# Kernel tuning notes

Measured on AMD Instinct MI355X. Metric: run time of the kernel, lower is better.

Reference implementation:

```python
import jax, jax.numpy as jnp
import numpy as np

N_BALLS = 256
BATCH = 128
N_STEPS = 100
MAX_EVENTS = 5
WORLD_W = 10.0
WORLD_H = 10.0
RADIUS = 0.1
HID = 64
DT = 0.05
INF = jnp.float32(1e30)

_II_np, _JJ_np = np.triu_indices(N_BALLS, 1)
_II = jnp.asarray(_II_np)
_JJ = jnp.asarray(_JJ_np)
# wall order: left, right, bottom, top (normals point into the box)
_WN = jnp.array([[1.0, 0.0], [-1.0, 0.0], [0.0, 1.0], [0.0, -1.0]], dtype=jnp.float32)
_WP = jnp.array([0.0, -WORLD_W, 0.0, -WORLD_H], dtype=jnp.float32)


def setup_inputs():
    key = jax.random.key(0)
    ks = jax.random.split(key, 6)
    pos = jax.random.uniform(ks[0], (BATCH, N_BALLS, 2), minval=0.5, maxval=9.5)
    vel = jax.random.normal(ks[1], (BATCH, N_BALLS, 2))
    state = jnp.concatenate([pos, vel], axis=-1)  # [B, N, 4]
    radii = jnp.full((N_BALLS,), RADIUS, dtype=jnp.float32)
    sc = 0.1
    W1 = jax.random.normal(ks[2], (HID, 2)) * sc
    b1 = jnp.zeros((HID,), jnp.float32)
    W2 = jax.random.normal(ks[3], (HID, HID)) * sc
    b2 = jnp.zeros((HID,), jnp.float32)
    W3 = jax.random.normal(ks[4], (1, HID)) * sc
    b3 = jnp.zeros((1,), jnp.float32)
    return {"state": state, "radii": radii, "W1": W1, "b1": b1, "W2": W2,
            "b2": b2, "W3": W3, "b3": b3, "dt": DT, "n_steps": N_STEPS}


def _detect(pos, vel, radii):
    # pos, vel: [N,2]; vectorized replacement of the Python O(N^2) loop.
    diff = pos[_JJ] - pos[_II]                       # [P,2]
    dist = jnp.linalg.norm(diff, axis=-1)            # [P]
    gap_b = dist - (radii[_II] + radii[_JJ])
    nhat = diff / (dist + 1e-8)[:, None]
    app_b = jnp.sum((vel[_JJ] - vel[_II]) * nhat, axis=-1)
    gb = jnp.where(app_b < 0, gap_b, INF)            # only approaching pairs
    r = radii
    gw = jnp.stack([pos[:, 0] - r, WORLD_W - pos[:, 0] - r,
                    pos[:, 1] - r, WORLD_H - pos[:, 1] - r], axis=-1)  # [N,4]
    vw = jnp.stack([vel[:, 0] < 0, vel[:, 0] > 0,
                    vel[:, 1] < 0, vel[:, 1] > 0], axis=-1)
    gw = jnp.where(vw, gw, INF)
    allg = jnp.concatenate([gb, gw.reshape(-1)])
    k = jnp.argmin(allg)
    P = gb.shape[0]
    is_ball = k < P
    gap = allg[k]
    bi = jnp.where(is_ball, k, 0)
    i_b, j_b = _II[bi], _JJ[bi]
    kw = jnp.where(is_ball, 0, k - P)
    i_w, wid = kw // 4, kw % 4
    return gap, is_ball, i_b, j_b, i_w, wid


def _apply_jump(s, i, j, W1, b1, W2, b2, W3, b3):
    pos, vel = s[..., :2], s[..., 2:]
    diff = pos[:, j] - pos[:, i]                               # [B,2]
    dist = jnp.maximum(jnp.linalg.norm(diff, axis=-1, keepdims=True), 1e-8)
    nhat = diff / dist
    app = jnp.sum((vel[:, j] - vel[:, i]) * nhat, axis=-1, keepdims=True)
    h = jnp.concatenate([dist, app], axis=-1)                  # [B,2]
    h = jax.nn.silu(h @ W1.T + b1)
    h = jax.nn.silu(h @ W2.T + b2)
    imp = (h @ W3.T + b3) * nhat                               # [B,2]
    vel_new = vel.at[:, i].add(imp).at[:, j].add(-imp)
    return jnp.concatenate([pos, vel_new], axis=-1)


def _apply_wall(s, i, wn, wp, r):
    pos, vel = s[..., :2], s[..., 2:]
    v, p = vel[:, i], pos[:, i]
    vn = jnp.sum(v * wn, axis=-1, keepdims=True)
    vel_new = vel.at[:, i].set(v - 2.0 * vn * wn)
    pn = jnp.sum(p * wn, axis=-1, keepdims=True)
    pen = jnp.maximum(wp + r - pn, 0.0)
    pos_new = pos.at[:, i].set(p + pen * wn)
    return jnp.concatenate([pos_new, vel_new], axis=-1)


def _rollout(state, radii, W1, b1, W2, b2, W3, b3, dt, n_steps):
    dt = jnp.float32(dt)

    def event_body(_, carry):
        curr, t_c, t_e, done = carry
        pos0, vel0 = curr[0, :, :2], curr[0, :, 2:]
        gap, is_ball, i_b, j_b, i_w, wid = _detect(pos0, vel0, radii)
        no_event = gap > 0.05
        n = pos0[j_b] - pos0[i_b]
        app_ball = -jnp.sum((vel0[j_b] - vel0[i_b]) * n / jnp.linalg.norm(n))
        app_wall = jnp.abs(jnp.max(vel0[i_w]))
        app = jnp.where(is_ball, app_ball, app_wall)
        t_ev = t_c + gap / jnp.maximum(app, 1e-6)
        # ZeroFlow is constant velocity -> dopri5 integrate is exact linear drift
        dte = jnp.where(t_ev > t_c + 1e-10, t_ev - t_c, 0.0)

        def apply_map(s):
            jm = _apply_jump(s, i_b, j_b, W1, b1, W2, b2, W3, b3)
            wm = _apply_wall(s, i_w, _WN[wid], _WP[wid], radii[i_w])
            return jnp.where(is_ball, jm, wm)

        state_a = apply_map(curr)                       # gap <= 0: jump now
        integ = curr.at[..., :2].add(curr[..., 2:] * dte)
        state_b = apply_map(integ)                      # 0 < gap: drift then jump
        act = (~done) & (~no_event)
        case_a = act & (gap <= 0)
        case_b = act & (gap > 0) & (app > 1e-6) & (t_ev < t_e)
        new_done = done | no_event | (act & (gap > 0) & ((app <= 1e-6) | (t_ev >= t_e)))
        new_curr = jnp.where(case_a, state_a, jnp.where(case_b, state_b, curr))
        new_t_c = jnp.where(case_b, t_ev, t_c)
        return new_curr, new_t_c, t_e, new_done

    def step(curr, step_idx):
        t_s = step_idx.astype(jnp.float32) * dt
        t_e = t_s + dt
        curr, t_c, _, _ = jax.lax.fori_loop(
            0, MAX_EVENTS, event_body, (curr, t_s, t_e, jnp.bool_(False)))
        dte = jnp.where(t_e > t_c + 1e-10, t_e - t_c, 0.0)
        curr = curr.at[..., :2].add(curr[..., 2:] * dte)
        return curr, curr

    _, traj = jax.lax.scan(step, state, jnp.arange(n_steps))
    return jnp.concatenate([state[None], traj], axis=0)   # [n_steps+1, B, N, 4]


def reference(state, radii, W1, b1, W2, b2, W3, b3, dt, n_steps):
    return _rollout(state, radii, W1, b1, W2, b2, W3, b3, dt, n_steps)
```

## Files before the change

kernel.cpp:

```cpp
#include <hip/hip_runtime.h>
#include <stdint.h>

#define NB 256
#define NBATCH 128
#define HID 64
#define MAXEV 5
#define MAXSTEPS 256
#define NT 43
#define NTILES 946
#define W2S 65
#define CAND_MAX 6144
#define CMARGIN 1.5f
#define NTHR 512
#define D2GATE 0.0626f

typedef unsigned long long u64;

__device__ __forceinline__ float bf2f(unsigned short u) {
    return __uint_as_float(((unsigned)u) << 16);
}
__device__ __forceinline__ unsigned short f2bf(float f) {
    unsigned u = __float_as_uint(f);
    u += 0x7FFFu + ((u >> 16) & 1u);
    return (unsigned short)(u >> 16);
}
__device__ __forceinline__ float rdin(const void* p, int idx, int bf) {
    return bf ? bf2f(((const unsigned short*)p)[idx]) : ((const float*)p)[idx];
}
__device__ __forceinline__ float silu_f(float x) {
    float s = __fdiv_rn(1.0f, __fadd_rn(1.0f, expf(-x)));
    return __fmul_rn(x, s);
}
__device__ __forceinline__ void lds_fence() {
    __builtin_amdgcn_wave_barrier();
    __threadfence_block();
    __builtin_amdgcn_wave_barrier();
}
__device__ __forceinline__ u64 shfl_down_u64(u64 v, int off) {
    unsigned lo = (unsigned)v, hi = (unsigned)(v >> 32);
    lo = __shfl_down(lo, off);
    hi = __shfl_down(hi, off);
    return (((u64)hi) << 32) | lo;
}
__device__ __forceinline__ unsigned fmap(float g) {
    unsigned u = __float_as_uint(g);
    unsigned m = (unsigned)(((int)u) >> 31) | 0x80000000u;
    return u ^ m;
}
__device__ __forceinline__ float funmap(unsigned sb) {
    unsigned u = (sb & 0x80000000u) ? (sb ^ 0x80000000u) : ~sb;
    return __uint_as_float(u);
}

__device__ __forceinline__ void append_agg(unsigned* list, int* counter, int cap, unsigned val) {
    u64 m = __ballot(1);
    int lane = (int)(threadIdx.x & 63);
    int ldr = (int)__builtin_ctzll(m);
    int pfx = (int)__builtin_popcountll(m & ((1ull << lane) - 1ull));
    int base = 0;
    if (lane == ldr) base = atomicAdd(counter, (int)__builtin_popcountll(m));
    base = __builtin_amdgcn_readfirstlane(base);
    int idx = base + pfx;
    if (idx < cap) list[idx] = val;
}

__device__ __forceinline__ u64 ball_key(const float4* ps, int i, int j,
                                        float dx, float dy, float d2,
                                        unsigned id, float rsum) {
    float4 A = ps[i], B = ps[j];
    float p1 = __fmul_rn(__fsub_rn(B.z, A.z), dx);
    float p2 = __fmul_rn(__fsub_rn(B.w, A.w), dy);
    float dot = __fadd_rn(p1, p2);
    float mag = __fadd_rn(fabsf(p1), fabsf(p2));
    bool appr;
    if (fabsf(dot) < __fmul_rn(1e-5f, mag)) {
        float dist = __fsqrt_rn(d2);
        float den = __fadd_rn(dist, 1e-8f);
        float ab = __fadd_rn(__fmul_rn(__fsub_rn(B.z, A.z), __fdiv_rn(dx, den)),
                             __fmul_rn(__fsub_rn(B.w, A.w), __fdiv_rn(dy, den)));
        appr = ab < 0.0f;
    } else {
        appr = dot < 0.0f;
    }
    if (!appr) return ~0ull;
    float gap = __fsub_rn(__fsqrt_rn(d2), rsum);
    return (((u64)fmap(gap)) << 17) | id;
}

__device__ void load_weights(float* w1, float* b1s, float* w2, float* b2s, float* w3, float* b3s,
                             const void* W1, const void* B1, const void* W2, const void* B2,
                             const void* W3, const void* B3, int bf, int tid, int nthr) {
    for (int k = tid; k < HID * 2; k += nthr) w1[k] = rdin(W1, k, bf);
    for (int k = tid; k < HID; k += nthr) {
        b1s[k] = rdin(B1, k, bf);
        b2s[k] = rdin(B2, k, bf);
        w3[k]  = rdin(W3, k, bf);
    }
    for (int k = tid; k < HID * HID; k += nthr) {
        int m = k >> 6, c = k & 63;
        w2[m * W2S + c] = rdin(W2, k, bf);
    }
    if (tid == 0) b3s[0] = rdin(B3, 0, bf);
}

__global__ void sniff_kernel(const unsigned short* st, int* ws) {
    __shared__ int ev;
    if (threadIdx.x == 0) ev = 0;
    __syncthreads();
    unsigned short u = st[threadIdx.x];
    int e = (u >> 7) & 0xFF;
    if (e >= 0x85) atomicOr(&ev, 1);
    __syncthreads();
    if (threadIdx.x == 0) ws[0] = ev ? 0 : 1;
}

__global__ void row0_kernel(const void* in, void* out, const int* ws) {
    int idx = blockIdx.x * blockDim.x + threadIdx.x;
    if (ws[0]) ((unsigned short*)out)[idx] = ((const unsigned short*)in)[idx];
    else       ((float*)out)[idx] = ((const float*)in)[idx];
}

__global__ __launch_bounds__(NTHR, 1) void sim_kernel(
    const void* in_state, const void* in_rad,
    const void* inW1, const void* inB1, const void* inW2, const void* inB2,
    const void* inW3, const void* inB3, const void* in_dt, const int* in_nsteps,
    void* out, const int* ws) {
    __shared__ float4 ps0[NB];
    __shared__ float4 psb[NB];
    __shared__ float2 pos2[NB];
    __shared__ float rad[NB];
    __shared__ float w1[HID * 2], b1s[HID], w2[HID * W2S], b2s[HID], w3s[HID], b3s[1];
    __shared__ float sc0[132], scb[132];
    __shared__ u64 redK[8];
    __shared__ float redF[4];
    __shared__ unsigned cand[CAND_MAX];
    __shared__ int candN;
    __shared__ int dI[4];
    __shared__ float dF[4];
    __shared__ int candF;
    __shared__ int rebF;

    int tid = threadIdx.x;
    int b = blockIdx.x;
    int bf = ws[0];

    if (tid < NB) {
        int base0 = tid * 4;
        float4 P;
        P.x = rdin(in_state, base0 + 0, bf);
        P.y = rdin(in_state, base0 + 1, bf);
        P.z = rdin(in_state, base0 + 2, bf);
        P.w = rdin(in_state, base0 + 3, bf);
        ps0[tid] = P;
        float2 p2v; p2v.x = P.x; p2v.y = P.y;
        pos2[tid] = p2v;
        int baseb = (b * NB + tid) * 4;
        float4 Q;
        Q.x = rdin(in_state, baseb + 0, bf);
        Q.y = rdin(in_state, baseb + 1, bf);
        Q.z = rdin(in_state, baseb + 2, bf);
        Q.w = rdin(in_state, baseb + 3, bf);
        psb[tid] = Q;
        rad[tid] = rdin(in_rad, tid, bf);
        float m2 = P.z * P.z + P.w * P.w;
        #pragma unroll
        for (int off = 32; off; off >>= 1) m2 = fmaxf(m2, __shfl_down(m2, off));
        if ((tid & 63) == 0) redF[tid >> 6] = m2;
    }
    load_weights(w1, b1s, w2, b2s, w3s, b3s, inW1, inB1, inW2, inB2, inW3, inB3, bf, tid, NTHR);
    if (tid == 0) { candN = 0; candF = 0; rebF = 1; }

    float dtv = rdin(in_dt, 0, bf);
    int NS = in_nsteps[0]; if (NS > MAXSTEPS) NS = MAXSTEPS; if (NS < 0) NS = 0;

    int i0a = -1, j0a = 0, i0b = -1, j0b = 0;
    {
        int T = tid;
        if (T < NTILES) {
            int rem = T, r = 0;
            while (rem >= NT - r) { rem -= NT - r; r++; }
            i0a = r * 6; j0a = (r + rem) * 6;
        }
        T = tid + NTHR;
        if (T < NTILES) {
            int rem = T, r = 0;
            while (rem >= NT - r) { rem -= NT - r; r++; }
            i0b = r * 6; j0b = (r + rem) * 6;
        }
    }
    __syncthreads();
    float rsum = __fadd_rn(rad[0], rad[0]);

    float thB = __fadd_rn(__fadd_rn(rsum, 0.05f), CMARGIN);
    float th2B = __fmul_rn(thB, thB);

    int nc = 0;
    bool candOvf = false;
    float used = 1e30f, vcap = 0.0f;

    for (int s = 0; s < NS; s++) {
        int rebuild = rebF;
        float t_s = __fmul_rn((float)s, dtv);
        float t_e = __fadd_rn(t_s, dtv);
        float t_c = t_s;
        if (tid < 64) {
            if (rebuild) {
                vcap = sqrtf(fmaxf(fmaxf(redF[0], redF[1]), fmaxf(redF[2], redF[3])));
                used = 0.0f;
            }
            used = __fadd_rn(used, __fmul_rn(__fmul_rn(2.0f, dtv), vcap));
            if (tid == 0 && rebuild) candF = 0;
        }

        for (int e = 0; e < MAXEV; e++) {
            u64 kC = ~0ull;
            bool fullscan = (e == 0) ? (rebuild != 0) : (candF != 0);
            bool doAppend = (e == 0) && rebuild;
            if (fullscan) {
                #pragma unroll
                for (int tt = 0; tt < 2; tt++) {
                    int I0 = tt ? i0b : i0a;
                    int J0 = tt ? j0b : j0a;
                    if (I0 < 0) continue;
                    float2 Pi[6], Pj[6];
                    #pragma unroll
                    for (int a = 0; a < 6; a++) {
                        int ii = I0 + a; ii = ii < NB ? ii : NB - 1;
                        int jj = J0 + a; jj = jj < NB ? jj : NB - 1;
                        Pi[a] = pos2[ii]; Pj[a] = pos2[jj];
                    }
                    #pragma unroll
                    for (int a = 0; a < 6; a++) {
                        int i = I0 + a;
                        #pragma unroll
                        for (int bb = 0; bb < 6; bb++) {
                            int j = J0 + bb;
                            bool ok = (i < NB) && (j < NB) && (j > i);
                            float dx = __fsub_rn(Pj[bb].x, Pi[a].x);
                            float dy = __fsub_rn(Pj[bb].y, Pi[a].y);
                            float d2 = __fadd_rn(__fmul_rn(dx, dx), __fmul_rn(dy, dy));
                            unsigned id = (unsigned)((i << 8) | j);
                            if (doAppend && ok && d2 < th2B)
                                append_agg(cand, &candN, CAND_MAX, id);
                            if (ok && d2 < D2GATE) {
                                u64 key = ball_key(ps0, i, j, dx, dy, d2, id, rsum);
                                kC = key < kC ? key : kC;
                            }
                        }
                    }
                }
            } else {
                for (int c = tid; c < nc; c += NTHR) {
                    unsigned id = cand[c];
                    int i = (int)(id >> 8), j = (int)(id & 255u);
                    float2 A = pos2[i], B = pos2[j];
                    float dx = __fsub_rn(B.x, A.x), dy = __fsub_rn(B.y, A.y);
                    float d2 = __fadd_rn(__fmul_rn(dx, dx), __fmul_rn(dy, dy));
                    if (d2 < D2GATE) {
                        u64 key = ball_key(ps0, i, j, dx, dy, d2, id, rsum);
                        kC = key < kC ? key : kC;
                    }
                }
            }
            {
                int ball = tid & 255, wsel = tid >> 8;
                float4 P = ps0[ball]; float r = rad[ball];
                #pragma unroll
                for (int q = 0; q < 2; q++) {
                    int w = wsel * 2 + q;
                    float g; bool valid;
                    if (w == 0)      { g = __fsub_rn(P.x, r); valid = P.z < 0.0f; }
                    else if (w == 1) { g = __fsub_rn(__fsub_rn(10.0f, P.x), r); valid = P.z > 0.0f; }
                    else if (w == 2) { g = __fsub_rn(P.y, r); valid = P.w < 0.0f; }
                    else             { g = __fsub_rn(__fsub_rn(10.0f, P.y), r); valid = P.w > 0.0f; }
                    if (valid) {
                        u64 key = (((u64)fmap(g)) << 17) | 0x10000u | (unsigned)(ball * 4 + w);
                        kC = key < kC ? key : kC;
                    }
                }
            }
            #pragma unroll
            for (int off = 32; off; off >>= 1) {
                u64 o = shfl_down_u64(kC, off);
                kC = o < kC ? o : kC;
            }
            if ((tid & 63) == 0) redK[tid >> 6] = kC;
            __syncthreads();

            if (e == 0 && rebuild) {
                int ct = candN;
                candOvf = ct > CAND_MAX;
                nc = candOvf ? CAND_MAX : ct;
            }

            float g_nx = 0, g_ny = 0, g_dist = 0, g_app = 0;
            float4 gA, gB;
            if (tid < 64) {
                u64 m = redK[0];
                #pragma unroll
                for (int q = 1; q < 8; q++) m = redK[q] < m ? redK[q] : m;
                int code_ = 0; float dteB_ = 0.0f, tcn_ = t_c;
                int ei_ = 0, ej_ = 0;
                if (m != ~0ull) {
                    bool is_ball = ((m >> 16) & 1ull) == 0;
                    unsigned id = (unsigned)(m & 0xFFFFull);
                    float gap = funmap((unsigned)(m >> 17));
                    int pi = (int)(id >> 8), pj = (int)(id & 255u);
                    int wb = (int)(id >> 2), ww = (int)(id & 3u);
                    ei_ = is_ball ? pi : wb;
                    ej_ = is_ball ? pj : ww;
                    if (!(gap > 0.05f)) {
                        float app;
                        if (is_ball) {
                            float4 A = ps0[pi], B = ps0[pj];
                            float dx = __fsub_rn(B.x, A.x), dy = __fsub_rn(B.y, A.y);
                            float nrm = __fsqrt_rn(__fadd_rn(__fmul_rn(dx, dx), __fmul_rn(dy, dy)));
                            float dvx = __fsub_rn(B.z, A.z), dvy = __fsub_rn(B.w, A.w);
                            app = -__fadd_rn(__fdiv_rn(__fmul_rn(dvx, dx), nrm),
                                             __fdiv_rn(__fmul_rn(dvy, dy), nrm));
                        } else {
                            float4 Wb = ps0[wb];
                            app = fabsf(fmaxf(Wb.z, Wb.w));
                        }
                        float t_ev = __fadd_rn(t_c, __fdiv_rn(gap, fmaxf(app, 1e-6f)));
                        if (gap <= 0.0f) {
                            code_ = is_ball ? 1 : 3;
                        } else if (app > 1e-6f && t_ev < t_e) {
                            code_ = is_ball ? 2 : 4;
                            dteB_ = (t_ev > __fadd_rn(t_c, 1e-10f)) ? __fsub_rn(t_ev, t_c) : 0.0f;
                            tcn_ = t_ev;
                        }
                    }
                }
                if (tid == 0) {
                    dI[0] = code_; dI[1] = ei_; dI[2] = ej_;
                    dF[0] = dteB_; dF[1] = tcn_;
                }
                if (code_ != 0 && code_ <= 2) {
                    float4 A = ps0[ei_], B = ps0[ej_];
                    if (code_ == 2) {
                        A.x = __fadd_rn(A.x, __fmul_rn(A.z, dteB_));
                        A.y = __fadd_rn(A.y, __fmul_rn(A.w, dteB_));
                        B.x = __fadd_rn(B.x, __fmul_rn(B.z, dteB_));
                        B.y = __fadd_rn(B.y, __fmul_rn(B.w, dteB_));
                    }
                    gA = A; gB = B;
                    float dx = __fsub_rn(B.x, A.x), dy = __fsub_rn(B.y, A.y);
                    float nrm = __fsqrt_rn(__fadd_rn(__fmul_rn(dx, dx), __fmul_rn(dy, dy)));
                    float dist = fmaxf(nrm, 1e-8f);
                    g_nx = __fdiv_rn(dx, dist); g_ny = __fdiv_rn(dy, dist);
                    g_dist = dist;
                    float dvx = __fsub_rn(B.z, A.z), dvy = __fsub_rn(B.w, A.w);
                    g_app = __fadd_rn(__fmul_rn(dvx, g_nx), __fmul_rn(dvy, g_ny));
                }
            }
            __syncthreads();

            int code = dI[0];
            if (code == 0) break;
            int ei = dI[1], ejw = dI[2];
            float dteB = dF[0];
            t_c = dF[1];
            bool integ = (code == 2) || (code == 4);

            if (code <= 2) {
                if (tid < 64) {
                    float a = __fadd_rn(__fadd_rn(__fmul_rn(g_dist, w1[2 * tid]),
                                                  __fmul_rn(g_app, w1[2 * tid + 1])), b1s[tid]);
                    sc0[4 + tid] = silu_f(a);
                    lds_fence();
                    float acc = 0.0f;
                    const float* row = &w2[tid * W2S];
                    #pragma unroll 8
                    for (int k = 0; k < HID; k++) acc = __fadd_rn(acc, __fmul_rn(sc0[4 + k], row[k]));
                    acc = __fadd_rn(acc, b2s[tid]);
                    sc0[68 + tid] = silu_f(acc);
                    lds_fence();
                    float acc3 = 0.0f;
                    #pragma unroll 8
                    for (int k = 0; k < HID; k++)
                        acc3 = __fadd_rn(acc3, __fmul_rn(sc0[68 + k], w3s[k]));
                    float impv = __fadd_rn(acc3, b3s[0]);
                    float ix = __fmul_rn(impv, g_nx), iy = __fmul_rn(impv, g_ny);
                    float nAz = __fadd_rn(gA.z, ix),  nAw = __fadd_rn(gA.w, iy);
                    float nBz = __fadd_rn(gB.z, -ix), nBw = __fadd_rn(gB.w, -iy);
                    if (tid == 0) {
                        float4 outA; outA.x = gA.x; outA.y = gA.y; outA.z = nAz; outA.w = nAw;
                        float4 outB; outB.x = gB.x; outB.y = gB.y; outB.z = nBz; outB.w = nBw;
                        ps0[ei] = outA; ps0[ejw] = outB;
                        float2 pa; pa.x = gA.x; pa.y = gA.y; pos2[ei] = pa;
                        float2 pb; pb.x = gB.x; pb.y = gB.y; pos2[ejw] = pb;
                    }
                    float s1 = sqrtf(nAz * nAz + nAw * nAw);
                    float s2 = sqrtf(nBz * nBz + nBw * nBw);
                    float nv = fmaxf(s1, s2);
                    used = __fadd_rn(used, __fmul_rn(__fmul_rn(2.0f, dtv),
                                                     fmaxf(__fsub_rn(nv, vcap), 0.0f)));
                    vcap = fmaxf(vcap, nv);
                    int nf = (candOvf || (__fadd_rn(used, 1e-3f) > CMARGIN)) ? 1 : 0;
                    if (tid == 0) candF = nf;
                } else if (tid < 128) {
                    int lane = tid - 64;
                    float4 A = psb[ei], B = psb[ejw];
                    if (integ) {
                        A.x = __fadd_rn(A.x, __fmul_rn(A.z, dteB));
                        A.y = __fadd_rn(A.y, __fmul_rn(A.w, dteB));
                        B.x = __fadd_rn(B.x, __fmul_rn(B.z, dteB));
                        B.y = __fadd_rn(B.y, __fmul_rn(B.w, dteB));
                    }
                    float dx = __fsub_rn(B.x, A.x), dy = __fsub_rn(B.y, A.y);
                    float nrm = __fsqrt_rn(__fadd_rn(__fmul_rn(dx, dx), __fmul_rn(dy, dy)));
                    float dist = fmaxf(nrm, 1e-8f);
                    float nx = __fdiv_rn(dx, dist), ny = __fdiv_rn(dy, dist);
                    float dvx = __fsub_rn(B.z, A.z), dvy = __fsub_rn(B.w, A.w);
                    float app2 = __fadd_rn(__fmul_rn(dvx, nx), __fmul_rn(dvy, ny));
                    float a = __fadd_rn(__fadd_rn(__fmul_rn(dist, w1[2 * lane]),
                                                  __fmul_rn(app2, w1[2 * lane + 1])), b1s[lane]);
                    scb[4 + lane] = silu_f(a);
                    lds_fence();
                    float acc = 0.0f;
                    const float* row = &w2[lane * W2S];
                    #pragma unroll 8
                    for (int k = 0; k < HID; k++) acc = __fadd_rn(acc, __fmul_rn(scb[4 + k], row[k]));
                    acc = __fadd_rn(acc, b2s[lane]);
                    scb[68 + lane] = silu_f(acc);
                    lds_fence();
                    float acc3 = 0.0f;
                    #pragma unroll 8
                    for (int k = 0; k < HID; k++)
                        acc3 = __fadd_rn(acc3, __fmul_rn(scb[68 + k], w3s[k]));
                    float impv = __fadd_rn(acc3, b3s[0]);
                    if (lane == 0) {
                        float ix = __fmul_rn(impv, nx), iy = __fmul_rn(impv, ny);
                        float4 outA; outA.x = A.x; outA.y = A.y;
                        outA.z = __fadd_rn(A.z, ix);  outA.w = __fadd_rn(A.w, iy);
                        float4 outB; outB.x = B.x; outB.y = B.y;
                        outB.z = __fadd_rn(B.z, -ix); outB.w = __fadd_rn(B.w, -iy);
                        psb[ei] = outA; psb[ejw] = outB;
                    }
                } else if (tid < 384) {
                    int t = tid - 128;
                    if (integ && t != ei && t != ejw) {
                        float4 P = ps0[t];
                        P.x = __fadd_rn(P.x, __fmul_rn(P.z, dteB));
                        P.y = __fadd_rn(P.y, __fmul_rn(P.w, dteB));
                        ps0[t] = P;
                        float2 pp; pp.x = P.x; pp.y = P.y; pos2[t] = pp;
                    }
                } else {
                    #pragma unroll
                    for (int q = 0; q < 2; q++) {
                        int t = (tid - 384) + q * 128;
                        if (integ && t != ei && t != ejw) {
                            float4 Q = psb[t];
                            Q.x = __fadd_rn(Q.x, __fmul_rn(Q.z, dteB));
                            Q.y = __fadd_rn(Q.y, __fmul_rn(Q.w, dteB));
                            psb[t] = Q;
                        }
                    }
                }
                __syncthreads();
            } else {
                const float wnx[4] = {1.f, -1.f, 0.f, 0.f};
                const float wny[4] = {0.f, 0.f, 1.f, -1.f};
                const float wpv[4] = {0.f, -10.f, 0.f, -10.f};
                int w = ejw;
                if (tid < 64) {
                    float4 P = ps0[ei];
                    if (integ) {
                        P.x = __fadd_rn(P.x, __fmul_rn(P.z, dteB));
                        P.y = __fadd_rn(P.y, __fmul_rn(P.w, dteB));
                    }
                    float vn = __fadd_rn(__fmul_rn(P.z, wnx[w]), __fmul_rn(P.w, wny[w]));
                    float t2 = __fmul_rn(2.0f, vn);
                    float nvx = __fsub_rn(P.z, __fmul_rn(t2, wnx[w]));
                    float nvy = __fsub_rn(P.w, __fmul_rn(t2, wny[w]));
                    float pn = __fadd_rn(__fmul_rn(P.x, wnx[w]), __fmul_rn(P.y, wny[w]));
                    float pen = fmaxf(__fsub_rn(__fadd_rn(wpv[w], rad[ei]), pn), 0.0f);
                    float4 nP;
                    nP.x = __fadd_rn(P.x, __fmul_rn(pen, wnx[w]));
                    nP.y = __fadd_rn(P.y, __fmul_rn(pen, wny[w]));
                    nP.z = nvx; nP.w = nvy;
                    used = __fadd_rn(used, pen);
                    int nf = (candOvf || (__fadd_rn(used, 1e-3f) > CMARGIN)) ? 1 : 0;
                    if (tid == 0) {
                        ps0[ei] = nP;
                        float2 pp; pp.x = nP.x; pp.y = nP.y; pos2[ei] = pp;
                        candF = nf;
                    }
                } else if (tid < 128) {
                    if (tid == 64) {
                        float4 P = psb[ei];
                        if (integ) {
                            P.x = __fadd_rn(P.x, __fmul_rn(P.z, dteB));
                            P.y = __fadd_rn(P.y, __fmul_rn(P.w, dteB));
                        }
                        float vn = __fadd_rn(__fmul_rn(P.z, wnx[w]), __fmul_rn(P.w, wny[w]));
                        float t2 = __fmul_rn(2.0f, vn);
                        float nvx = __fsub_rn(P.z, __fmul_rn(t2, wnx[w]));
                        float nvy = __fsub_rn(P.w, __fmul_rn(t2, wny[w]));
                        float pn = __fadd_rn(__fmul_rn(P.x, wnx[w]), __fmul_rn(P.y, wny[w]));
                        float pen = fmaxf(__fsub_rn(__fadd_rn(wpv[w], rad[ei]), pn), 0.0f);
                        float4 nP;
                        nP.x = __fadd_rn(P.x, __fmul_rn(pen, wnx[w]));
                        nP.y = __fadd_rn(P.y, __fmul_rn(pen, wny[w]));
                        nP.z = nvx; nP.w = nvy;
                        psb[ei] = nP;
                    }
                } else if (tid < 384) {
                    int t = tid - 128;
                    if (integ && t != ei) {
                        float4 P = ps0[t];
                        P.x = __fadd_rn(P.x, __fmul_rn(P.z, dteB));
                        P.y = __fadd_rn(P.y, __fmul_rn(P.w, dteB));
                        ps0[t] = P;
                        float2 pp; pp.x = P.x; pp.y = P.y; pos2[t] = pp;
                    }
                } else {
                    #pragma unroll
                    for (int q = 0; q < 2; q++) {
                        int t = (tid - 384) + q * 128;
                        if (integ && t != ei) {
                            float4 Q = psb[t];
                            Q.x = __fadd_rn(Q.x, __fmul_rn(Q.z, dteB));
                            Q.y = __fadd_rn(Q.y, __fmul_rn(Q.w, dteB));
                            psb[t] = Q;
                        }
                    }
                }
                __syncthreads();
            }
        }

        float fd = (t_e > __fadd_rn(t_c, 1e-10f)) ? __fsub_rn(t_e, t_c) : 0.0f;
        if (tid < NB) {
            float4 P = ps0[tid];
            P.x = __fadd_rn(P.x, __fmul_rn(P.z, fd));
            P.y = __fadd_rn(P.y, __fmul_rn(P.w, fd));
            ps0[tid] = P;
            float2 pp; pp.x = P.x; pp.y = P.y; pos2[tid] = pp;
            float m2 = P.z * P.z + P.w * P.w;
            #pragma unroll
            for (int off = 32; off; off >>= 1) m2 = fmaxf(m2, __shfl_down(m2, off));
            if ((tid & 63) == 0) redF[tid >> 6] = m2;
            if (tid == 0) {
                candN = 0;
                float usedNext = __fadd_rn(used, __fmul_rn(__fmul_rn(2.0f, dtv), vcap));
                rebF = (candOvf || (__fadd_rn(usedNext, 1e-3f) > CMARGIN)) ? 1 : 0;
            }
        } else {
            int t = tid - NB;
            float4 Q = psb[t];
            Q.x = __fadd_rn(Q.x, __fmul_rn(Q.z, fd));
            Q.y = __fadd_rn(Q.y, __fmul_rn(Q.w, fd));
            psb[t] = Q;
            long long base = ((long long)(s + 1) * NBATCH + b) * (NB * 4);
            if (bf) {
                ushort4 v;
                v.x = f2bf(Q.x); v.y = f2bf(Q.y); v.z = f2bf(Q.z); v.w = f2bf(Q.w);
                ((ushort4*)((unsigned short*)out + base))[t] = v;
            } else {
                ((float4*)((float*)out + base))[t] = Q;
            }
        }
        __syncthreads();
    }
}

extern "C" void kernel_launch(void* const* d_in, const int* in_sizes, int n_in,
                              void* d_out, int out_size, void* d_ws, size_t ws_size,
                              hipStream_t stream) {
    int* ws = (int*)d_ws;
    sniff_kernel<<<1, 256, 0, stream>>>((const unsigned short*)d_in[0], ws);
    row0_kernel<<<(NBATCH * NB * 4) / 256, 256, 0, stream>>>(d_in[0], d_out, ws);
    sim_kernel<<<NBATCH, NTHR, 0, stream>>>(
        d_in[0], d_in[1], d_in[2], d_in[3], d_in[4], d_in[5], d_in[6], d_in[7],
        d_in[8], (const int*)d_in[9], d_out, ws);
}
```

Measured before the change: 3.317 ms.

## Run event loop in a single wavefront to remove block-wide barriers

The per-step event loop now runs entirely inside wave 0 (64 threads). It uses wave-level reductions, readlane broadcasts and an LDS fence in place of the __syncthreads-separated multi-wave phases. The rebuild full scan with candidate append is hoisted out of the event loop and done once per step by the whole block. MLP weights move from shared memory into registers, and per-ball radii are replaced by a single scalar. This cuts the many block barriers per event, but leaves 448 threads idle during events and makes one wave do all candidate and integration work.

Measured after the change: 11.77 ms. 3.55x slower.

```diff
diff --git a/kernel.cpp b/kernel.cpp
--- a/kernel.cpp
+++ b/kernel.cpp
@@ -8,7 +8,6 @@
 #define MAXSTEPS 256
 #define NT 43
 #define NTILES 946
-#define W2S 65
 #define CAND_MAX 6144
 #define CMARGIN 1.5f
 #define NTHR 512
@@ -50,6 +49,14 @@
 __device__ __forceinline__ float funmap(unsigned sb) {
     unsigned u = (sb & 0x80000000u) ? (sb ^ 0x80000000u) : ~sb;
     return __uint_as_float(u);
+}
+__device__ __forceinline__ float rlane(float v, int k) {
+    return __int_as_float(__builtin_amdgcn_readlane(__float_as_int(v), k));
+}
+__device__ __forceinline__ u64 bcast0_u64(u64 v) {
+    unsigned lo = (unsigned)__builtin_amdgcn_readlane((int)(unsigned)v, 0);
+    unsigned hi = (unsigned)__builtin_amdgcn_readlane((int)(unsigned)(v >> 32), 0);
+    return (((u64)hi) << 32) | lo;
 }
 
 __device__ __forceinline__ void append_agg(unsigned* list, int* counter, int cap, unsigned val) {
@@ -87,22 +94,6 @@
     return (((u64)fmap(gap)) << 17) | id;
 }
 
-__device__ void load_weights(float* w1, float* b1s, float* w2, float* b2s, float* w3, float* b3s,
-                             const void* W1, const void* B1, const void* W2, const void* B2,
-                             const void* W3, const void* B3, int bf, int tid, int nthr) {
-    for (int k = tid; k < HID * 2; k += nthr) w1[k] = rdin(W1, k, bf);
-    for (int k = tid; k < HID; k += nthr) {
-        b1s[k] = rdin(B1, k, bf);
-        b2s[k] = rdin(B2, k, bf);
-        w3[k]  = rdin(W3, k, bf);
-    }
-    for (int k = tid; k < HID * HID; k += nthr) {
-        int m = k >> 6, c = k & 63;
-        w2[m * W2S + c] = rdin(W2, k, bf);
-    }
-    if (tid == 0) b3s[0] = rdin(B3, 0, bf);
-}
-
 __global__ void sniff_kernel(const unsigned short* st, int* ws) {
     __shared__ int ev;
     if (threadIdx.x == 0) ev = 0;
@@ -128,16 +119,11 @@
     __shared__ float4 ps0[NB];
     __shared__ float4 psb[NB];
     __shared__ float2 pos2[NB];
-    __shared__ float rad[NB];
-    __shared__ float w1[HID * 2], b1s[HID], w2[HID * W2S], b2s[HID], w3s[HID], b3s[1];
-    __shared__ float sc0[132], scb[132];
     __shared__ u64 redK[8];
     __shared__ float redF[4];
     __shared__ unsigned cand[CAND_MAX];
     __shared__ int candN;
-    __shared__ int dI[4];
-    __shared__ float dF[4];
-    __shared__ int candF;
+    __shared__ float dFtc;
     __shared__ int rebF;
 
     int tid = threadIdx.x;
@@ -161,17 +147,30 @@
         Q.z = rdin(in_state, baseb + 2, bf);
         Q.w = rdin(in_state, baseb + 3, bf);
         psb[tid] = Q;
-        rad[tid] = rdin(in_rad, tid, bf);
         float m2 = P.z * P.z + P.w * P.w;
         #pragma unroll
         for (int off = 32; off; off >>= 1) m2 = fmaxf(m2, __shfl_down(m2, off));
         if ((tid & 63) == 0) redF[tid >> 6] = m2;
     }
-    load_weights(w1, b1s, w2, b2s, w3s, b3s, inW1, inB1, inW2, inB2, inW3, inB3, bf, tid, NTHR);
-    if (tid == 0) { candN = 0; candF = 0; rebF = 1; }
+    if (tid == 0) { candN = 0; rebF = 1; }
 
     float dtv = rdin(in_dt, 0, bf);
     int NS = in_nsteps[0]; if (NS > MAXSTEPS) NS = MAXSTEPS; if (NS < 0) NS = 0;
+    float rad0 = rdin(in_rad, 0, bf);
+    float rsum = __fadd_rn(rad0, rad0);
+
+    float w1a = 0.f, w1b = 0.f, b1r = 0.f, b2r = 0.f, w3r = 0.f, b3r = 0.f;
+    float w2row[HID];
+    if (tid < 64) {
+        w1a = rdin(inW1, 2 * tid, bf);
+        w1b = rdin(inW1, 2 * tid + 1, bf);
+        b1r = rdin(inB1, tid, bf);
+        b2r = rdin(inB2, tid, bf);
+        w3r = rdin(inW3, tid, bf);
+        b3r = rdin(inB3, 0, bf);
+        #pragma unroll
+        for (int k = 0; k < HID; k++) w2row[k] = rdin(inW2, tid * HID + k, bf);
+    }
 
     int i0a = -1, j0a = 0, i0b = -1, j0b = 0;
     {
@@ -189,13 +188,12 @@
         }
     }
     __syncthreads();
-    float rsum = __fadd_rn(rad[0], rad[0]);
 
     float thB = __fadd_rn(__fadd_rn(rsum, 0.05f), CMARGIN);
     float th2B = __fmul_rn(thB, thB);
 
     int nc = 0;
-    bool candOvf = false;
+    bool candOvf = false, candF = false;
     float used = 1e30f, vcap = 0.0f;
 
     for (int s = 0; s < NS; s++) {
@@ -203,112 +201,151 @@
         float t_s = __fmul_rn((float)s, dtv);
         float t_e = __fadd_rn(t_s, dtv);
         float t_c = t_s;
+
+        if (rebuild) {
+            u64 kC = ~0ull;
+            #pragma unroll
+            for (int tt = 0; tt < 2; tt++) {
+                int I0 = tt ? i0b : i0a;
+                int J0 = tt ? j0b : j0a;
+                if (I0 < 0) continue;
+                float2 Pi[6], Pj[6];
+                #pragma unroll
+                for (int a = 0; a < 6; a++) {
+                    int ii = I0 + a; ii = ii < NB ? ii : NB - 1;
+                    int jj = J0 + a; jj = jj < NB ? jj : NB - 1;
+                    Pi[a] = pos2[ii]; Pj[a] = pos2[jj];
+                }
+                #pragma unroll
+                for (int a = 0; a < 6; a++) {
+                    int i = I0 + a;
+                    #pragma unroll
+                    for (int bb = 0; bb < 6; bb++) {
+                        int j = J0 + bb;
+                        bool ok = (i < NB) && (j < NB) && (j > i);
+                        float dx = __fsub_rn(Pj[bb].x, Pi[a].x);
+                        float dy = __fsub_rn(Pj[bb].y, Pi[a].y);
+                        float d2 = __fadd_rn(__fmul_rn(dx, dx), __fmul_rn(dy, dy));
+                        unsigned id = (unsigned)((i << 8) | j);
+                        if (ok && d2 < th2B)
+                            append_agg(cand, &candN, CAND_MAX, id);
+                        if (ok && d2 < D2GATE) {
+                            u64 key = ball_key(ps0, i, j, dx, dy, d2, id, rsum);
+                            kC = key < kC ? key : kC;
+                        }
+                    }
+                }
+            }
+            {
+                int ball = tid & 255, wsel = tid >> 8;
+                float4 P = ps0[ball];
+                #pragma unroll
+                for (int q = 0; q < 2; q++) {
+                    int w = wsel * 2 + q;
+                    float g; bool valid;
+                    if (w == 0)      { g = __fsub_rn(P.x, rad0); valid = P.z < 0.0f; }
+                    else if (w == 1) { g = __fsub_rn(__fsub_rn(10.0f, P.x), rad0); valid = P.z > 0.0f; }
+                    else if (w == 2) { g = __fsub_rn(P.y, rad0); valid = P.w < 0.0f; }
+                    else             { g = __fsub_rn(__fsub_rn(10.0f, P.y), rad0); valid = P.w > 0.0f; }
+                    if (valid) {
+                        u64 key = (((u64)fmap(g)) << 17) | 0x10000u | (unsigned)(ball * 4 + w);
+                        kC = key < kC ? key : kC;
+                    }
+                }
+            }
+            #pragma unroll
+            for (int off = 32; off; off >>= 1) {
+                u64 o = shfl_down_u64(kC, off);
+                kC = o < kC ? o : kC;
+            }
+            if ((tid & 63) == 0) redK[tid >> 6] = kC;
+            __syncthreads();
+        }
+
         if (tid < 64) {
             if (rebuild) {
                 vcap = sqrtf(fmaxf(fmaxf(redF[0], redF[1]), fmaxf(redF[2], redF[3])));
                 used = 0.0f;
+                candF = false;
+                int ct = candN;
+                candOvf = ct > CAND_MAX;
+                nc = candOvf ? CAND_MAX : ct;
             }
             used = __fadd_rn(used, __fmul_rn(__fmul_rn(2.0f, dtv), vcap));
-            if (tid == 0 && rebuild) candF = 0;
-        }
-
-        for (int e = 0; e < MAXEV; e++) {
-            u64 kC = ~0ull;
-            bool fullscan = (e == 0) ? (rebuild != 0) : (candF != 0);
-            bool doAppend = (e == 0) && rebuild;
-            if (fullscan) {
-                #pragma unroll
-                for (int tt = 0; tt < 2; tt++) {
-                    int I0 = tt ? i0b : i0a;
-                    int J0 = tt ? j0b : j0a;
-                    if (I0 < 0) continue;
-                    float2 Pi[6], Pj[6];
+
+            for (int e = 0; e < MAXEV; e++) {
+                u64 m;
+                if (e == 0 && rebuild) {
+                    m = redK[0];
                     #pragma unroll
-                    for (int a = 0; a < 6; a++) {
-                        int ii = I0 + a; ii = ii < NB ? ii : NB - 1;
-                        int jj = J0 + a; jj = jj < NB ? jj : NB - 1;
-                        Pi[a] = pos2[ii]; Pj[a] = pos2[jj];
-                    }
-                    #pragma unroll
-                    for (int a = 0; a < 6; a++) {
-                        int i = I0 + a;
-                        #pragma unroll
-                        for (int bb = 0; bb < 6; bb++) {
-                            int j = J0 + bb;
-                            bool ok = (i < NB) && (j < NB) && (j > i);
-                            float dx = __fsub_rn(Pj[bb].x, Pi[a].x);
-                            float dy = __fsub_rn(Pj[bb].y, Pi[a].y);
+                    for (int q = 1; q < 8; q++) m = redK[q] < m ? redK[q] : m;
+                } else {
+                    u64 kC = ~0ull;
+                    if (candF) {
+                        for (int i = 0; i < NB - 1; i++) {
+                            float2 A = pos2[i];
+                            for (int jj = tid; jj < NB - 1 - i; jj += 64) {
+                                int j = i + 1 + jj;
+                                float2 Bp = pos2[j];
+                                float dx = __fsub_rn(Bp.x, A.x), dy = __fsub_rn(Bp.y, A.y);
+                                float d2 = __fadd_rn(__fmul_rn(dx, dx), __fmul_rn(dy, dy));
+                                if (d2 < D2GATE) {
+                                    unsigned id = (unsigned)((i << 8) | j);
+                                    u64 key = ball_key(ps0, i, j, dx, dy, d2, id, rsum);
+                                    kC = key < kC ? key : kC;
+                                }
+                            }
+                        }
+                    } else {
+                        for (int c = tid; c < nc; c += 64) {
+                            unsigned id = cand[c];
+                            int i = (int)(id >> 8), j = (int)(id & 255u);
+                            float2 A = pos2[i], Bp = pos2[j];
+                            float dx = __fsub_rn(Bp.x, A.x), dy = __fsub_rn(Bp.y, A.y);
                             float d2 = __fadd_rn(__fmul_rn(dx, dx), __fmul_rn(dy, dy));
-                            unsigned id = (unsigned)((i << 8) | j);
-                            if (doAppend && ok && d2 < th2B)
-                                append_agg(cand, &candN, CAND_MAX, id);
-                            if (ok && d2 < D2GATE) {
+                            if (d2 < D2GATE) {
                                 u64 key = ball_key(ps0, i, j, dx, dy, d2, id, rsum);
                                 kC = key < kC ? key : kC;
                             }
                         }
                     }
+                    #pragma unroll
+                    for (int q = 0; q < 4; q++) {
+                        int ball = tid + q * 64;
+                        float4 P = ps0[ball];
+                        #pragma unroll
+                        for (int w = 0; w < 4; w++) {
+                            float g; bool valid;
+                            if (w == 0)      { g = __fsub_rn(P.x, rad0); valid = P.z < 0.0f; }
+                            else if (w == 1) { g = __fsub_rn(__fsub_rn(10.0f, P.x), rad0); valid = P.z > 0.0f; }
+                            else if (w == 2) { g = __fsub_rn(P.y, rad0); valid = P.w < 0.0f; }
+                            else             { g = __fsub_rn(__fsub_rn(10.0f, P.y), rad0); valid = P.w > 0.0f; }
+                            if (valid) {
+                                u64 key = (((u64)fmap(g)) << 17) | 0x10000u | (unsigned)(ball * 4 + w);
+                                kC = key < kC ? key : kC;
+                            }
+                        }
+                    }
+                    #pragma unroll
+                    for (int off = 32; off; off >>= 1) {
+                        u64 o = shfl_down_u64(kC, off);
+                        kC = o < kC ? o : kC;
+                    }
+                    m = bcast0_u64(kC);
                 }
-            } else {
-                for (int c = tid; c < nc; c += NTHR) {
-                    unsigned id = cand[c];
-                    int i = (int)(id >> 8), j = (int)(id & 255u);
-                    float2 A = pos2[i], B = pos2[j];
-                    float dx = __fsub_rn(B.x, A.x), dy = __fsub_rn(B.y, A.y);
-                    float d2 = __fadd_rn(__fmul_rn(dx, dx), __fmul_rn(dy, dy));
-                    if (d2 < D2GATE) {
-                        u64 key = ball_key(ps0, i, j, dx, dy, d2, id, rsum);
-                        kC = key < kC ? key : kC;
-                    }
-                }
-            }
-            {
-                int ball = tid & 255, wsel = tid >> 8;
-                float4 P = ps0[ball]; float r = rad[ball];
-                #pragma unroll
-                for (int q = 0; q < 2; q++) {
-                    int w = wsel * 2 + q;
-                    float g; bool valid;
-                    if (w == 0)      { g = __fsub_rn(P.x, r); valid = P.z < 0.0f; }
-                    else if (w == 1) { g = __fsub_rn(__fsub_rn(10.0f, P.x), r); valid = P.z > 0.0f; }
-                    else if (w == 2) { g = __fsub_rn(P.y, r); valid = P.w < 0.0f; }
-                    else             { g = __fsub_rn(__fsub_rn(10.0f, P.y), r); valid = P.w > 0.0f; }
-                    if (valid) {
-                        u64 key = (((u64)fmap(g)) << 17) | 0x10000u | (unsigned)(ball * 4 + w);
-                        kC = key < kC ? key : kC;
-                    }
-                }
-            }
-            #pragma unroll
-            for (int off = 32; off; off >>= 1) {
-                u64 o = shfl_down_u64(kC, off);
-                kC = o < kC ? o : kC;
-            }
-            if ((tid & 63) == 0) redK[tid >> 6] = kC;
-            __syncthreads();
-
-            if (e == 0 && rebuild) {
-                int ct = candN;
-                candOvf = ct > CAND_MAX;
-                nc = candOvf ? CAND_MAX : ct;
-            }
-
-            float g_nx = 0, g_ny = 0, g_dist = 0, g_app = 0;
-            float4 gA, gB;
-            if (tid < 64) {
-                u64 m = redK[0];
-                #pragma unroll
-                for (int q = 1; q < 8; q++) m = redK[q] < m ? redK[q] : m;
-                int code_ = 0; float dteB_ = 0.0f, tcn_ = t_c;
-                int ei_ = 0, ej_ = 0;
+
+                float g_nx = 0, g_ny = 0, g_dist = 0, g_app = 0;
+                float4 gA, gB;
+                int code = 0; float dteB = 0.0f; float tcn = t_c;
+                int ei = 0, ejw = 0;
                 if (m != ~0ull) {
                     bool is_ball = ((m >> 16) & 1ull) == 0;
                     unsigned id = (unsigned)(m & 0xFFFFull);
                     float gap = funmap((unsigned)(m >> 17));
                     int pi = (int)(id >> 8), pj = (int)(id & 255u);
                     int wb = (int)(id >> 2), ww = (int)(id & 3u);
-                    ei_ = is_ball ? pi : wb;
-                    ej_ = is_ball ? pj : ww;
+                    ei = is_ball ? pi : wb;
+                    ejw = is_ball ? pj : ww;
                     if (!(gap > 0.05f)) {
                         float app;
                         if (is_ball) {
@@ -324,72 +361,90 @@
                         }
                         float t_ev = __fadd_rn(t_c, __fdiv_rn(gap, fmaxf(app, 1e-6f)));
                         if (gap <= 0.0f) {
-                            code_ = is_ball ? 1 : 3;
+                            code = is_ball ? 1 : 3;
                         } else if (app > 1e-6f && t_ev < t_e) {
-                            code_ = is_ball ? 2 : 4;
-                            dteB_ = (t_ev > __fadd_rn(t_c, 1e-10f)) ? __fsub_rn(t_ev, t_c) : 0.0f;
-                            tcn_ = t_ev;
+                            code = is_ball ? 2 : 4;
+                            dteB = (t_ev > __fadd_rn(t_c, 1e-10f)) ? __fsub_rn(t_ev, t_c) : 0.0f;
+                            tcn = t_ev;
                         }
                     }
                 }
-                if (tid == 0) {
-                    dI[0] = code_; dI[1] = ei_; dI[2] = ej_;
-                    dF[0] = dteB_; dF[1] = tcn_;
-                }
-                if (code_ != 0 && code_ <= 2) {
-                    float4 A = ps0[ei_], B = ps0[ej_];
-                    if (code_ == 2) {
-                        A.x = __fadd_rn(A.x, __fmul_rn(A.z, dteB_));
-                        A.y = __fadd_rn(A.y, __fmul_rn(A.w, dteB_));
-                        B.x = __fadd_rn(B.x, __fmul_rn(B.z, dteB_));
-                        B.y = __fadd_rn(B.y, __fmul_rn(B.w, dteB_));
-                    }
-                    gA = A; gB = B;
-                    float dx = __fsub_rn(B.x, A.x), dy = __fsub_rn(B.y, A.y);
-                    float nrm = __fsqrt_rn(__fadd_rn(__fmul_rn(dx, dx), __fmul_rn(dy, dy)));
-                    float dist = fmaxf(nrm, 1e-8f);
-                    g_nx = __fdiv_rn(dx, dist); g_ny = __fdiv_rn(dy, dist);
-                    g_dist = dist;
-                    float dvx = __fsub_rn(B.z, A.z), dvy = __fsub_rn(B.w, A.w);
-                    g_app = __fadd_rn(__fmul_rn(dvx, g_nx), __fmul_rn(dvy, g_ny));
-                }
-            }
-            __syncthreads();
-
-            int code = dI[0];
-            if (code == 0) break;
-            int ei = dI[1], ejw = dI[2];
-            float dteB = dF[0];
-            t_c = dF[1];
-            bool integ = (code == 2) || (code == 4);
-
-            if (code <= 2) {
-                if (tid < 64) {
-                    float a = __fadd_rn(__fadd_rn(__fmul_rn(g_dist, w1[2 * tid]),
-                                                  __fmul_rn(g_app, w1[2 * tid + 1])), b1s[tid]);
-                    sc0[4 + tid] = silu_f(a);
-                    lds_fence();
-                    float acc = 0.0f;
-                    const float* row = &w2[tid * W2S];
-                    #pragma unroll 8
-                    for (int k = 0; k < HID; k++) acc = __fadd_rn(acc, __fmul_rn(sc0[4 + k], row[k]));
-                    acc = __fadd_rn(acc, b2s[tid]);
-                    sc0[68 + tid] = silu_f(acc);
-                    lds_fence();
-                    float acc3 = 0.0f;
-                    #pragma unroll 8
-                    for (int k = 0; k < HID; k++)
-                        acc3 = __fadd_rn(acc3, __fmul_rn(sc0[68 + k], w3s[k]));
-                    float impv = __fadd_rn(acc3, b3s[0]);
-                    float ix = __fmul_rn(impv, g_nx), iy = __fmul_rn(impv, g_ny);
+                if (code == 0) break;
+                t_c = tcn;
+                bool integ = (code == 2) || (code == 4);
+
+                if (code <= 2) {
+                    {
+                        float4 A = ps0[ei], B = ps0[ejw];
+                        if (code == 2) {
+                            A.x = __fadd_rn(A.x, __fmul_rn(A.z, dteB));
+                            A.y = __fadd_rn(A.y, __fmul_rn(A.w, dteB));
+                            B.x = __fadd_rn(B.x, __fmul_rn(B.z, dteB));
+                            B.y = __fadd_rn(B.y, __fmul_rn(B.w, dteB));
+                        }
+                        gA = A; gB = B;
+                        float dx = __fsub_rn(B.x, A.x), dy = __fsub_rn(B.y, A.y);
+                        float nrm = __fsqrt_rn(__fadd_rn(__fmul_rn(dx, dx), __fmul_rn(dy, dy)));
+                        float dist = fmaxf(nrm, 1e-8f);
+                        g_nx = __fdiv_rn(dx, dist); g_ny = __fdiv_rn(dy, dist);
+                        g_dist = dist;
+                        float dvx = __fsub_rn(B.z, A.z), dvy = __fsub_rn(B.w, A.w);
+                        g_app = __fadd_rn(__fmul_rn(dvx, g_nx), __fmul_rn(dvy, g_ny));
+                    }
+                    float4 Ab = psb[ei], Bb = psb[ejw];
+                    if (integ) {
+                        Ab.x = __fadd_rn(Ab.x, __fmul_rn(Ab.z, dteB));
+                        Ab.y = __fadd_rn(Ab.y, __fmul_rn(Ab.w, dteB));
+                        Bb.x = __fadd_rn(Bb.x, __fmul_rn(Bb.z, dteB));
+                        Bb.y = __fadd_rn(Bb.y, __fmul_rn(Bb.w, dteB));
+                    }
+                    float dxb = __fsub_rn(Bb.x, Ab.x), dyb = __fsub_rn(Bb.y, Ab.y);
+                    float nrmb = __fsqrt_rn(__fadd_rn(__fmul_rn(dxb, dxb), __fmul_rn(dyb, dyb)));
+                    float distb = fmaxf(nrmb, 1e-8f);
+                    float nxb = __fdiv_rn(dxb, distb), nyb = __fdiv_rn(dyb, distb);
+                    float dvxb = __fsub_rn(Bb.z, Ab.z), dvyb = __fsub_rn(Bb.w, Ab.w);
+                    float appb = __fadd_rn(__fmul_rn(dvxb, nxb), __fmul_rn(dvyb, nyb));
+
+                    float h1_0 = silu_f(__fadd_rn(__fadd_rn(__fmul_rn(g_dist, w1a),
+                                                            __fmul_rn(g_app, w1b)), b1r));
+                    float h1_b = silu_f(__fadd_rn(__fadd_rn(__fmul_rn(distb, w1a),
+                                                            __fmul_rn(appb, w1b)), b1r));
+                    float a0 = 0.0f, ab2 = 0.0f;
+                    #pragma unroll
+                    for (int k = 0; k < HID; k++) {
+                        float s0 = rlane(h1_0, k);
+                        float sb = rlane(h1_b, k);
+                        a0  = __fadd_rn(a0,  __fmul_rn(s0, w2row[k]));
+                        ab2 = __fadd_rn(ab2, __fmul_rn(sb, w2row[k]));
+                    }
+                    float h2_0 = silu_f(__fadd_rn(a0, b2r));
+                    float h2_b = silu_f(__fadd_rn(ab2, b2r));
+                    float pw0 = __fmul_rn(h2_0, w3r);
+                    float pwb = __fmul_rn(h2_b, w3r);
+                    float s30 = 0.0f, s3b = 0.0f;
+                    #pragma unroll
+                    for (int k = 0; k < HID; k++) {
+                        s30 = __fadd_rn(s30, rlane(pw0, k));
+                        s3b = __fadd_rn(s3b, rlane(pwb, k));
+                    }
+                    float imp0 = __fadd_rn(s30, b3r);
+                    float impb = __fadd_rn(s3b, b3r);
+
+                    float ix = __fmul_rn(imp0, g_nx), iy = __fmul_rn(imp0, g_ny);
                     float nAz = __fadd_rn(gA.z, ix),  nAw = __fadd_rn(gA.w, iy);
                     float nBz = __fadd_rn(gB.z, -ix), nBw = __fadd_rn(gB.w, -iy);
                     if (tid == 0) {
-                        float4 outA; outA.x = gA.x; outA.y = gA.y; outA.z = nAz; outA.w = nAw;
-                        float4 outB; outB.x = gB.x; outB.y = gB.y; outB.z = nBz; outB.w = nBw;
-                        ps0[ei] = outA; ps0[ejw] = outB;
+                        float4 oA; oA.x = gA.x; oA.y = gA.y; oA.z = nAz; oA.w = nAw;
+                        float4 oB; oB.x = gB.x; oB.y = gB.y; oB.z = nBz; oB.w = nBw;
+                        ps0[ei] = oA; ps0[ejw] = oB;
                         float2 pa; pa.x = gA.x; pa.y = gA.y; pos2[ei] = pa;
                         float2 pb; pb.x = gB.x; pb.y = gB.y; pos2[ejw] = pb;
+                        float ixb = __fmul_rn(impb, nxb), iyb = __fmul_rn(impb, nyb);
+                        float4 qA; qA.x = Ab.x; qA.y = Ab.y;
+                        qA.z = __fadd_rn(Ab.z, ixb);  qA.w = __fadd_rn(Ab.w, iyb);
+                        float4 qB; qB.x = Bb.x; qB.y = Bb.y;
+                        qB.z = __fadd_rn(Bb.z, -ixb); qB.w = __fadd_rn(Bb.w, -iyb);
+                        psb[ei] = qA; psb[ejw] = qB;
                     }
                     float s1 = sqrtf(nAz * nAz + nAw * nAw);
                     float s2 = sqrtf(nBz * nBz + nBw * nBw);
@@ -397,100 +452,33 @@
                     used = __fadd_rn(used, __fmul_rn(__fmul_rn(2.0f, dtv),
                                                      fmaxf(__fsub_rn(nv, vcap), 0.0f)));
                     vcap = fmaxf(vcap, nv);
-                    int nf = (candOvf || (__fadd_rn(used, 1e-3f) > CMARGIN)) ? 1 : 0;
-                    if (tid == 0) candF = nf;
-                } else if (tid < 128) {
-                    int lane = tid - 64;
-                    float4 A = psb[ei], B = psb[ejw];
+                    candF = candOvf || (__fadd_rn(used, 1e-3f) > CMARGIN);
+
                     if (integ) {
-                        A.x = __fadd_rn(A.x, __fmul_rn(A.z, dteB));
-                        A.y = __fadd_rn(A.y, __fmul_rn(A.w, dteB));
-                        B.x = __fadd_rn(B.x, __fmul_rn(B.z, dteB));
-                        B.y = __fadd_rn(B.y, __fmul_rn(B.w, dteB));
-                    }
-                    float dx = __fsub_rn(B.x, A.x), dy = __fsub_rn(B.y, A.y);
-                    float nrm = __fsqrt_rn(__fadd_rn(__fmul_rn(dx, dx), __fmul_rn(dy, dy)));
-                    float dist = fmaxf(nrm, 1e-8f);
-                    float nx = __fdiv_rn(dx, dist), ny = __fdiv_rn(dy, dist);
-                    float dvx = __fsub_rn(B.z, A.z), dvy = __fsub_rn(B.w, A.w);
-                    float app2 = __fadd_rn(__fmul_rn(dvx, nx), __fmul_rn(dvy, ny));
-                    float a = __fadd_rn(__fadd_rn(__fmul_rn(dist, w1[2 * lane]),
-                                                  __fmul_rn(app2, w1[2 * lane + 1])), b1s[lane]);
-                    scb[4 + lane] = silu_f(a);
-                    lds_fence();
-                    float acc = 0.0f;
-                    const float* row = &w2[lane * W2S];
-                    #pragma unroll 8
-                    for (int k = 0; k < HID; k++) acc = __fadd_rn(acc, __fmul_rn(scb[4 + k], row[k]));
-                    acc = __fadd_rn(acc, b2s[lane]);
-                    scb[68 + lane] = silu_f(acc);
-                    lds_fence();
-                    float acc3 = 0.0f;
-                    #pragma unroll 8
-                    for (int k = 0; k < HID; k++)
-                        acc3 = __fadd_rn(acc3, __fmul_rn(scb[68 + k], w3s[k]));
-                    float impv = __fadd_rn(acc3, b3s[0]);
-                    if (lane == 0) {
-                        float ix = __fmul_rn(impv, nx), iy = __fmul_rn(impv, ny);
-                        float4 outA; outA.x = A.x; outA.y = A.y;
-                        outA.z = __fadd_rn(A.z, ix);  outA.w = __fadd_rn(A.w, iy);
-                        float4 outB; outB.x = B.x; outB.y = B.y;
-                        outB.z = __fadd_rn(B.z, -ix); outB.w = __fadd_rn(B.w, -iy);
-                        psb[ei] = outA; psb[ejw] = outB;
-                    }
-                } else if (tid < 384) {
-                    int t = tid - 128;
-                    if (integ && t != ei && t != ejw) {
-                        float4 P = ps0[t];
-                        P.x = __fadd_rn(P.x, __fmul_rn(P.z, dteB));
-                        P.y = __fadd_rn(P.y, __fmul_rn(P.w, dteB));
-                        ps0[t] = P;
-                        float2 pp; pp.x = P.x; pp.y = P.y; pos2[t] = pp;
+                        #pragma unroll
+                        for (int q = 0; q < 4; q++) {
+                            int t = tid + q * 64;
+                            if (t != ei && t != ejw) {
+                                float4 P = ps0[t];
+                                P.x = __fadd_rn(P.x, __fmul_rn(P.z, dteB));
+                                P.y = __fadd_rn(P.y, __fmul_rn(P.w, dteB));
+                                ps0[t] = P;
+                                float2 pp; pp.x = P.x; pp.y = P.y; pos2[t] = pp;
+                                float4 Q = psb[t];
+                                Q.x = __fadd_rn(Q.x, __fmul_rn(Q.z, dteB));
+                                Q.y = __fadd_rn(Q.y, __fmul_rn(Q.w, dteB));
+                                psb[t] = Q;
+                            }
+                        }
                     }
                 } else {
-                    #pragma unroll
-                    for (int q = 0; q < 2; q++) {
-                        int t = (tid - 384) + q * 128;
-                        if (integ && t != ei && t != ejw) {
-                            float4 Q = psb[t];
-                            Q.x = __fadd_rn(Q.x, __fmul_rn(Q.z, dteB));
-                            Q.y = __fadd_rn(Q.y, __fmul_rn(Q.w, dteB));
-                            psb[t] = Q;
-                        }
-                    }
-                }
-                __syncthreads();
-            } else {
-                const float wnx[4] = {1.f, -1.f, 0.f, 0.f};
-                const float wny[4] = {0.f, 0.f, 1.f, -1.f};
-                const float wpv[4] = {0.f, -10.f, 0.f, -10.f};
-                int w = ejw;
-                if (tid < 64) {
-                    float4 P = ps0[ei];
-                    if (integ) {
-                        P.x = __fadd_rn(P.x, __fmul_rn(P.z, dteB));
-                        P.y = __fadd_rn(P.y, __fmul_rn(P.w, dteB));
-                    }
-                    float vn = __fadd_rn(__fmul_rn(P.z, wnx[w]), __fmul_rn(P.w, wny[w]));
-                    float t2 = __fmul_rn(2.0f, vn);
-                    float nvx = __fsub_rn(P.z, __fmul_rn(t2, wnx[w]));
-                    float nvy = __fsub_rn(P.w, __fmul_rn(t2, wny[w]));
-                    float pn = __fadd_rn(__fmul_rn(P.x, wnx[w]), __fmul_rn(P.y, wny[w]));
-                    float pen = fmaxf(__fsub_rn(__fadd_rn(wpv[w], rad[ei]), pn), 0.0f);
-                    float4 nP;
-                    nP.x = __fadd_rn(P.x, __fmul_rn(pen, wnx[w]));
-                    nP.y = __fadd_rn(P.y, __fmul_rn(pen, wny[w]));
-                    nP.z = nvx; nP.w = nvy;
-                    used = __fadd_rn(used, pen);
-                    int nf = (candOvf || (__fadd_rn(used, 1e-3f) > CMARGIN)) ? 1 : 0;
-                    if (tid == 0) {
-                        ps0[ei] = nP;
-                        float2 pp; pp.x = nP.x; pp.y = nP.y; pos2[ei] = pp;
-                        candF = nf;
-                    }
-                } else if (tid < 128) {
-                    if (tid == 64) {
-                        float4 P = psb[ei];
+                    const float wnx[4] = {1.f, -1.f, 0.f, 0.f};
+                    const float wny[4] = {0.f, 0.f, 1.f, -1.f};
+                    const float wpv[4] = {0.f, -10.f, 0.f, -10.f};
+                    int w = ejw;
+                    float pen;
+                    {
+                        float4 P = ps0[ei];
                         if (integ) {
                             P.x = __fadd_rn(P.x, __fmul_rn(P.z, dteB));
                             P.y = __fadd_rn(P.y, __fmul_rn(P.w, dteB));
@@ -500,39 +488,63 @@
                         float nvx = __fsub_rn(P.z, __fmul_rn(t2, wnx[w]));
                         float nvy = __fsub_rn(P.w, __fmul_rn(t2, wny[w]));
                         float pn = __fadd_rn(__fmul_rn(P.x, wnx[w]), __fmul_rn(P.y, wny[w]));
-                        float pen = fmaxf(__fsub_rn(__fadd_rn(wpv[w], rad[ei]), pn), 0.0f);
+                        pen = fmaxf(__fsub_rn(__fadd_rn(wpv[w], rad0), pn), 0.0f);
                         float4 nP;
                         nP.x = __fadd_rn(P.x, __fmul_rn(pen, wnx[w]));
                         nP.y = __fadd_rn(P.y, __fmul_rn(pen, wny[w]));
                         nP.z = nvx; nP.w = nvy;
-                        psb[ei] = nP;
-                    }
-                } else if (tid < 384) {
-                    int t = tid - 128;
-                    if (integ && t != ei) {
-                        float4 P = ps0[t];
-                        P.x = __fadd_rn(P.x, __fmul_rn(P.z, dteB));
-                        P.y = __fadd_rn(P.y, __fmul_rn(P.w, dteB));
-                        ps0[t] = P;
-                        float2 pp; pp.x = P.x; pp.y = P.y; pos2[t] = pp;
-                    }
-                } else {
-                    #pragma unroll
-                    for (int q = 0; q < 2; q++) {
-                        int t = (tid - 384) + q * 128;
-                        if (integ && t != ei) {
-                            float4 Q = psb[t];
-                            Q.x = __fadd_rn(Q.x, __fmul_rn(Q.z, dteB));
-                            Q.y = __fadd_rn(Q.y, __fmul_rn(Q.w, dteB));
-                            psb[t] = Q;
+                        if (tid == 0) {
+                            ps0[ei] = nP;
+                            float2 pp; pp.x = nP.x; pp.y = nP.y; pos2[ei] = pp;
+                        }
+                    }
+                    {
+                        float4 P = psb[ei];
+                        if (integ) {
+                            P.x = __fadd_rn(P.x, __fmul_rn(P.z, dteB));
+                            P.y = __fadd_rn(P.y, __fmul_rn(P.w, dteB));
+                        }
+                        float vn = __fadd_rn(__fmul_rn(P.z, wnx[w]), __fmul_rn(P.w, wny[w]));
+                        float t2 = __fmul_rn(2.0f, vn);
+                        float nvx = __fsub_rn(P.z, __fmul_rn(t2, wnx[w]));
+                        float nvy = __fsub_rn(P.w, __fmul_rn(t2, wny[w]));
+                        float pn = __fadd_rn(__fmul_rn(P.x, wnx[w]), __fmul_rn(P.y, wny[w]));
+                        float pen2 = fmaxf(__fsub_rn(__fadd_rn(wpv[w], rad0), pn), 0.0f);
+                        float4 nP;
+                        nP.x = __fadd_rn(P.x, __fmul_rn(pen2, wnx[w]));
+                        nP.y = __fadd_rn(P.y, __fmul_rn(pen2, wny[w]));
+                        nP.z = nvx; nP.w = nvy;
+                        if (tid == 0) psb[ei] = nP;
+                    }
+                    used = __fadd_rn(used, pen);
+                    candF = candOvf || (__fadd_rn(used, 1e-3f) > CMARGIN);
+
+                    if (integ) {
+                        #pragma unroll
+                        for (int q = 0; q < 4; q++) {
+                            int t = tid + q * 64;
+                            if (t != ei) {
+                                float4 P = ps0[t];
+                                P.x = __fadd_rn(P.x, __fmul_rn(P.z, dteB));
+                                P.y = __fadd_rn(P.y, __fmul_rn(P.w, dteB));
+                                ps0[t] = P;
+                                float2 pp; pp.x = P.x; pp.y = P.y; pos2[t] = pp;
+                                float4 Q = psb[t];
+                                Q.x = __fadd_rn(Q.x, __fmul_rn(Q.z, dteB));
+                                Q.y = __fadd_rn(Q.y, __fmul_rn(Q.w, dteB));
+                                psb[t] = Q;
+                            }
                         }
                     }
                 }
-                __syncthreads();
-            }
+                lds_fence();
+            }
+            if (tid == 0) dFtc = t_c;
         }
-
-        float fd = (t_e > __fadd_rn(t_c, 1e-10f)) ? __fsub_rn(t_e, t_c) : 0.0f;
+        __syncthreads();
+
+        float tcf = dFtc;
+        float fd = (t_e > __fadd_rn(tcf, 1e-10f)) ? __fsub_rn(t_e, tcf) : 0.0f;
         if (tid < NB) {
             float4 P = ps0[tid];
             P.x = __fadd_rn(P.x, __fmul_rn(P.z, fd));
```
